# Performance work log

Hardware: AMD Instinct MI355X
Metric: run time of the kernel (lower is better)

Reference implementation:

```python
import jax, jax.numpy as jnp
import numpy as np

P, N, GRID, C, S, STEPS, N_ADJ = 128, 512, 112, 64, 128, 3, 4
HW = GRID * GRID
IN_DIM = C + 2


def _ring_adjacency():
    # prepare_gcn_component builds a ring graph: each vertex connected to
    # n_adj nearest neighbors along the polygon, row-normalized.
    offs = np.concatenate([np.arange(1, N_ADJ // 2 + 1), -np.arange(1, N_ADJ // 2 + 1)])
    A = np.zeros((N, N), np.float32)
    idx = np.arange(N)
    for o in offs:
        A[idx, (idx + o) % N] = 1.0
    A /= A.sum(1, keepdims=True)
    return jnp.asarray(A)


def setup_inputs() -> dict:
    key = jax.random.key(0)
    ks = jax.random.split(key, 10)
    std = 0.01  # matches m.weight.data.normal_(0.0, 0.01)
    return {
        "feature": jax.random.normal(ks[0], (P, HW, C), jnp.float32),
        "init_polys": jax.random.uniform(ks[1], (P, N, 2), jnp.float32),
        "adj": _ring_adjacency(),
        "W1s": jax.random.normal(ks[2], (STEPS, IN_DIM, S), jnp.float32) * std,
        "W1n": jax.random.normal(ks[3], (STEPS, IN_DIM, S), jnp.float32) * std,
        "b1": jnp.zeros((STEPS, S), jnp.float32),
        "W2s": jax.random.normal(ks[4], (STEPS, S, S), jnp.float32) * std,
        "W2n": jax.random.normal(ks[5], (STEPS, S, S), jnp.float32) * std,
        "b2": jnp.zeros((STEPS, S), jnp.float32),
        "Wfc": jax.random.normal(ks[6], (STEPS, S, 2), jnp.float32) * std,
        "bfc": jnp.zeros((STEPS, 2), jnp.float32),
    }


def _gather(feat, ids):
    # feat: [P, HW, C], ids: [P, N] int -> [P, N, C]
    return jnp.take_along_axis(feat, ids[:, :, None], axis=1)


def _nearest_sample(feature, poly):
    # step-0 `sampling` path: gather at floor(coord*grid) flat indices
    X0 = jnp.clip(jnp.floor(poly[..., 0] * GRID), 0, GRID - 1)
    Y0 = jnp.clip(jnp.floor(poly[..., 1] * GRID), 0, GRID - 1)
    ids = (X0 + Y0 * GRID).astype(jnp.int32)
    return _gather(feature, ids)


def _interpolated_sum(feature, poly):
    Xs = poly[..., 0] * GRID
    Ys = poly[..., 1] * GRID
    X0 = jnp.floor(Xs); X1 = X0 + 1.0
    Y0 = jnp.floor(Ys); Y1 = Y0 + 1.0
    w00 = (X1 - Xs) * (Y1 - Ys)
    w01 = (X1 - Xs) * (Ys - Y0)
    w10 = (Xs - X0) * (Y1 - Ys)
    w11 = (Xs - X0) * (Ys - Y0)
    X0c = jnp.clip(X0, 0, GRID - 1).astype(jnp.int32)
    X1c = jnp.clip(X1, 0, GRID - 1).astype(jnp.int32)
    Y0c = jnp.clip(Y0, 0, GRID - 1).astype(jnp.int32)
    Y1c = jnp.clip(Y1, 0, GRID - 1).astype(jnp.int32)
    M00 = _gather(feature, X0c + Y0c * GRID)
    M01 = _gather(feature, X0c + Y1c * GRID)
    M10 = _gather(feature, X1c + Y0c * GRID)
    M11 = _gather(feature, X1c + Y1c * GRID)
    return (w00[..., None] * M00 + w01[..., None] * M01 +
            w10[..., None] * M10 + w11[..., None] * M11)


def _gconv(x, adj, Ws, Wn, b):
    # x: [P, N, D]; adj: [N, N] (shared ring graph)
    nbr = jnp.einsum('nm,pmd->pnd', adj, x)
    return x @ Ws + nbr @ Wn + b


def _gcn(x, adj, i, W1s, W1n, b1, W2s, W2n, b2, Wfc, bfc):
    h = jax.nn.relu(_gconv(x, adj, W1s[i], W1n[i], b1[i]))
    h = jax.nn.relu(_gconv(h, adj, W2s[i], W2n[i], b2[i]))
    return h @ Wfc[i] + bfc[i]  # [P, N, 2]


def reference(feature, init_polys, adj, W1s, W1n, b1, W2s, W2n, b2, Wfc, bfc):
    poly = init_polys
    for i in range(STEPS):
        cnn_feat = _nearest_sample(feature, poly) if i == 0 else _interpolated_sum(feature, poly)
        inp = jnp.concatenate([cnn_feat, poly], axis=2)  # [P, N, C+2]
        pred = _gcn(inp, adj, i, W1s, W1n, b1, W2s, W2n, b2, Wfc, bfc)
        poly = poly + pred
    return poly
```

## Files before the change

### kernel.cpp

```cpp
#include <hip/hip_runtime.h>

#define P_      128
#define NV      512
#define GRID_   112
#define HW_     (GRID_*GRID_)
#define C_      64
#define S_      128

typedef short bf16x8 __attribute__((ext_vector_type(8)));
typedef float f32x4  __attribute__((ext_vector_type(4)));

__device__ __forceinline__ unsigned short f2bf(float x) {
    union { float f; unsigned int u; } v; v.f = x;
    unsigned int r = (v.u + 0x7FFFu + ((v.u >> 16) & 1u)) >> 16;
    return (unsigned short)r;
}
__device__ __forceinline__ float2 up2(unsigned int u) {
    union { unsigned int u; float f; } a, b;
    a.u = u << 16; b.u = u & 0xFFFF0000u;
    return make_float2(a.f, b.f);
}
__device__ __forceinline__ unsigned int pk2(float lo, float hi) {
    return (unsigned int)f2bf(lo) | ((unsigned int)f2bf(hi) << 16);
}

__global__ __launch_bounds__(256) void wprep_kernel(
    const float* __restrict__ W1s, const float* __restrict__ W1n,
    const float* __restrict__ W2s, const float* __restrict__ W2n,
    unsigned short* __restrict__ W1p, unsigned short* __restrict__ W2p)
{
    int idx = blockIdx.x * 256 + threadIdx.x;
    const int N1 = 3 * 5 * 8 * 64 * 8;
    const int N2 = 3 * 8 * 8 * 64 * 8;
    if (idx < N1) {
        int j = idx & 7, lane = (idx >> 3) & 63, nt = (idx >> 9) & 7;
        int ks = (idx >> 12) % 5, step = idx / 20480;
        int n = nt * 16 + (lane & 15);
        int k = ks * 32 + (lane >> 4) * 8 + j;
        float v = 0.f;
        if (k < 66)       v = W1s[(step * 66 + k) * 128 + n];
        else if (k < 132) v = W1n[(step * 66 + (k - 66)) * 128 + n];
        W1p[idx] = f2bf(v);
    } else if (idx < N1 + N2) {
        int e = idx - N1;
        int j = e & 7, lane = (e >> 3) & 63, nt = (e >> 9) & 7;
        int ks = (e >> 12) & 7, step = e >> 15;
        int n = nt * 16 + (lane & 15);
        int k = ks * 32 + (lane >> 4) * 8 + j;
        float v = (k < 128) ? W2s[(step * 128 + k) * 128 + n]
                            : W2n[(step * 128 + (k - 128)) * 128 + n];
        W2p[e] = f2bf(v);
    }
}

__global__ __launch_bounds__(256) void sample_kernel(
    const float* __restrict__ feature, const float* __restrict__ poly,
    unsigned short* __restrict__ inp, int nearest)
{
    int w = threadIdx.x >> 6, lane = threadIdx.x & 63;
    int g = blockIdx.x * 4 + w;
    int p = g >> 9;
    float px = poly[2 * g], py = poly[2 * g + 1];
    const float* fb = feature + (size_t)p * HW_ * C_;
    float val;
    if (nearest) {
        float X0 = fminf(fmaxf(floorf(px * (float)GRID_), 0.f), (float)(GRID_ - 1));
        float Y0 = fminf(fmaxf(floorf(py * (float)GRID_), 0.f), (float)(GRID_ - 1));
        int id = (int)X0 + (int)Y0 * GRID_;
        val = fb[(size_t)id * C_ + lane];
    } else {
        float Xs = px * (float)GRID_, Ys = py * (float)GRID_;
        float X0 = floorf(Xs), Y0 = floorf(Ys);
        float X1 = X0 + 1.f, Y1 = Y0 + 1.f;
        float ax = X1 - Xs, bx = Xs - X0;
        float ay = Y1 - Ys, by = Ys - Y0;
        int X0c = (int)fminf(fmaxf(X0, 0.f), (float)(GRID_ - 1));
        int X1c = (int)fminf(fmaxf(X1, 0.f), (float)(GRID_ - 1));
        int Y0c = (int)fminf(fmaxf(Y0, 0.f), (float)(GRID_ - 1));
        int Y1c = (int)fminf(fmaxf(Y1, 0.f), (float)(GRID_ - 1));
        float m00 = fb[(size_t)(X0c + Y0c * GRID_) * C_ + lane];
        float m01 = fb[(size_t)(X0c + Y1c * GRID_) * C_ + lane];
        float m10 = fb[(size_t)(X1c + Y0c * GRID_) * C_ + lane];
        float m11 = fb[(size_t)(X1c + Y1c * GRID_) * C_ + lane];
        val = (ax * ay) * m00 + (ax * by) * m01 + (bx * ay) * m10 + (bx * by) * m11;
    }
    unsigned short* row = inp + (size_t)g * 72;
    row[lane] = f2bf(val);
    if (lane < 8)
        row[64 + lane] = (lane == 0) ? f2bf(px) : (lane == 1) ? f2bf(py) : 0;
}

__global__ __launch_bounds__(256) void gcn_kernel(
    const unsigned short* __restrict__ inp,
    const unsigned short* __restrict__ W1p,
    const float* __restrict__ b1,
    const unsigned short* __restrict__ W2p,
    const float* __restrict__ b2,
    const float* __restrict__ Wfc, const float* __restrict__ bfc,
    const float* __restrict__ poly_in, float* __restrict__ poly_out)
{
    __shared__ __align__(16) char smem[54400];
    unsigned int*   raw_u = (unsigned int*)smem;
    unsigned int*   A1_u  = (unsigned int*)(smem + 10368);
    unsigned short* h1s   = (unsigned short*)smem;
    unsigned int*   A2_u  = (unsigned int*)(smem + 21120);
    float*          h2    = (float*)(smem + 21120);

    int p = blockIdx.x >> 3, n0 = (blockIdx.x & 7) * 64;
    int wv = threadIdx.x >> 6, lane = threadIdx.x & 63;
    int m = lane & 15, q = lane >> 4;

    const unsigned int* inpu = (const unsigned int*)inp + (size_t)p * NV * 36;
    for (int idx = threadIdx.x; idx < 72 * 36; idx += 256) {
        int r = idx / 36, u = idx - r * 36;
        raw_u[idx] = inpu[(size_t)((n0 + r - 4) & 511) * 36 + u];
    }
    __syncthreads();

    for (int idx = threadIdx.x; idx < 80 * 84; idx += 256) {
        int a = idx / 84, u = idx - a * 84;
        unsigned int val = 0u;
        if (a < 68) {
            if (u < 33) {
                val = raw_u[(a + 2) * 36 + u];
            } else if (u < 66) {
                int uu = u - 33;
                float2 fa = up2(raw_u[a * 36 + uu]),       fb2 = up2(raw_u[(a + 1) * 36 + uu]);
                float2 fc = up2(raw_u[(a + 3) * 36 + uu]), fd  = up2(raw_u[(a + 4) * 36 + uu]);
                val = pk2(0.25f * (fa.x + fb2.x + fc.x + fd.x),
                          0.25f * (fa.y + fb2.y + fc.y + fd.y));
            }
        }
        A1_u[idx] = val;
    }
    __syncthreads();

    f32x4 acc1[10];
    #pragma unroll
    for (int i = 0; i < 10; i++) acc1[i] = (f32x4){0.f, 0.f, 0.f, 0.f};
    const bf16x8* B1 = (const bf16x8*)W1p;
    #pragma unroll
    for (int i = 0; i < 10; i++) {
        int t = wv * 10 + i;
        int mt = t >> 3, nt = t & 7;
        const unsigned short* arow = (const unsigned short*)A1_u + (mt * 16 + m) * 168 + q * 8;
        #pragma unroll
        for (int ks = 0; ks < 5; ks++) {
            bf16x8 a = *(const bf16x8*)(arow + ks * 32);
            bf16x8 b = B1[(ks * 8 + nt) * 64 + lane];
            acc1[i] = __builtin_amdgcn_mfma_f32_16x16x32_bf16(a, b, acc1[i], 0, 0, 0);
        }
    }
    __syncthreads();

    #pragma unroll
    for (int i = 0; i < 10; i++) {
        int t = wv * 10 + i;
        int mt = t >> 3, nt = t & 7;
        int col = nt * 16 + m;
        float bias = b1[col];
        #pragma unroll
        for (int rg = 0; rg < 4; rg++) {
            int row = mt * 16 + q * 4 + rg;
            h1s[row * 132 + col] = f2bf(fmaxf(acc1[i][rg] + bias, 0.f));
        }
    }
    __syncthreads();

    const unsigned int* h1u = (const unsigned int*)h1s;
    for (int idx = threadIdx.x; idx < 64 * 128; idx += 256) {
        int a = idx >> 7, u = idx & 127;
        unsigned int val;
        if (u < 64) {
            val = h1u[(a + 2) * 66 + u];
        } else {
            int uu = u - 64;
            float2 fa = up2(h1u[a * 66 + uu]),       fb2 = up2(h1u[(a + 1) * 66 + uu]);
            float2 fc = up2(h1u[(a + 3) * 66 + uu]), fd  = up2(h1u[(a + 4) * 66 + uu]);
            val = pk2(0.25f * (fa.x + fb2.x + fc.x + fd.x),
                      0.25f * (fa.y + fb2.y + fc.y + fd.y));
        }
        A2_u[a * 130 + u] = val;
    }
    __syncthreads();

    f32x4 acc2[8];
    #pragma unroll
    for (int nt = 0; nt < 8; nt++) acc2[nt] = (f32x4){0.f, 0.f, 0.f, 0.f};
    const bf16x8* B2 = (const bf16x8*)W2p;
    const unsigned short* arow2 = (const unsigned short*)A2_u + (wv * 16 + m) * 260 + q * 8;
    #pragma unroll
    for (int ks = 0; ks < 8; ks++) {
        bf16x8 a = *(const bf16x8*)(arow2 + ks * 32);
        #pragma unroll
        for (int nt = 0; nt < 8; nt++) {
            bf16x8 b = B2[(ks * 8 + nt) * 64 + lane];
            acc2[nt] = __builtin_amdgcn_mfma_f32_16x16x32_bf16(a, b, acc2[nt], 0, 0, 0);
        }
    }
    __syncthreads();

    #pragma unroll
    for (int nt = 0; nt < 8; nt++) {
        int col = nt * 16 + m;
        float bias = b2[col];
        #pragma unroll
        for (int rg = 0; rg < 4; rg++) {
            int row = wv * 16 + q * 4 + rg;
            h2[row * 129 + col] = fmaxf(acc2[nt][rg] + bias, 0.f);
        }
    }
    __syncthreads();

    {
        int t = threadIdx.x;
        int oi = t >> 1, half = t & 1;
        int v = oi >> 1, j = oi & 1;
        float pr = half ? 0.f : bfc[j];
        const float* hv = h2 + v * 129 + half * 64;
        #pragma unroll 8
        for (int cc = 0; cc < 64; cc++)
            pr += hv[cc] * Wfc[(half * 64 + cc) * 2 + j];
        pr += __shfl_xor(pr, 1);
        if (half == 0) {
            size_t o = ((size_t)p * NV + n0 + v) * 2 + j;
            poly_out[o] = poly_in[o] + pr;
        }
    }
}

extern "C" void kernel_launch(void* const* d_in, const int* in_sizes, int n_in,
                              void* d_out, int out_size, void* d_ws, size_t ws_size,
                              hipStream_t stream)
{
    const float* feature    = (const float*)d_in[0];
    const float* init_polys = (const float*)d_in[1];
    const float* W1s = (const float*)d_in[3];
    const float* W1n = (const float*)d_in[4];
    const float* b1  = (const float*)d_in[5];
    const float* W2s = (const float*)d_in[6];
    const float* W2n = (const float*)d_in[7];
    const float* b2  = (const float*)d_in[8];
    const float* Wfc = (const float*)d_in[9];
    const float* bfc = (const float*)d_in[10];
    float* out = (float*)d_out;

    char* wsb = (char*)d_ws;
    float* polyA = (float*)wsb;                  wsb += (size_t)P_ * NV * 2 * 4;
    float* polyB = (float*)wsb;                  wsb += (size_t)P_ * NV * 2 * 4;
    unsigned short* W1p = (unsigned short*)wsb;  wsb += (size_t)61440 * 2;
    unsigned short* W2p = (unsigned short*)wsb;  wsb += (size_t)98304 * 2;
    unsigned short* inp = (unsigned short*)wsb;

    wprep_kernel<<<624, 256, 0, stream>>>(W1s, W1n, W2s, W2n, W1p, W2p);

    const float* pin = init_polys;
    for (int i = 0; i < 3; i++) {
        float* pout = (i == 2) ? out : ((i == 0) ? polyA : polyB);
        sample_kernel<<<P_ * NV / 4, 256, 0, stream>>>(feature, pin, inp, i == 0);
        gcn_kernel<<<P_ * 8, 256, 0, stream>>>(
            inp, W1p + (size_t)i * 20480, b1 + i * 128,
            W2p + (size_t)i * 32768, b2 + i * 128,
            Wfc + i * 256, bfc + i * 2,
            pin, pout);
        pin = pout;
    }
}
```

Measured before the change: 644.7 us.

## Fuse feature sampling into GCN kernel and reorganize MFMA tiling by column pairs

```diff
diff --git a/kernel.cpp b/kernel.cpp
--- a/kernel.cpp
+++ b/kernel.cpp
@@ -53,53 +53,18 @@
     }
 }
 
-__global__ __launch_bounds__(256) void sample_kernel(
-    const float* __restrict__ feature, const float* __restrict__ poly,
-    unsigned short* __restrict__ inp, int nearest)
-{
-    int w = threadIdx.x >> 6, lane = threadIdx.x & 63;
-    int g = blockIdx.x * 4 + w;
-    int p = g >> 9;
-    float px = poly[2 * g], py = poly[2 * g + 1];
-    const float* fb = feature + (size_t)p * HW_ * C_;
-    float val;
-    if (nearest) {
-        float X0 = fminf(fmaxf(floorf(px * (float)GRID_), 0.f), (float)(GRID_ - 1));
-        float Y0 = fminf(fmaxf(floorf(py * (float)GRID_), 0.f), (float)(GRID_ - 1));
-        int id = (int)X0 + (int)Y0 * GRID_;
-        val = fb[(size_t)id * C_ + lane];
-    } else {
-        float Xs = px * (float)GRID_, Ys = py * (float)GRID_;
-        float X0 = floorf(Xs), Y0 = floorf(Ys);
-        float X1 = X0 + 1.f, Y1 = Y0 + 1.f;
-        float ax = X1 - Xs, bx = Xs - X0;
-        float ay = Y1 - Ys, by = Ys - Y0;
-        int X0c = (int)fminf(fmaxf(X0, 0.f), (float)(GRID_ - 1));
-        int X1c = (int)fminf(fmaxf(X1, 0.f), (float)(GRID_ - 1));
-        int Y0c = (int)fminf(fmaxf(Y0, 0.f), (float)(GRID_ - 1));
-        int Y1c = (int)fminf(fmaxf(Y1, 0.f), (float)(GRID_ - 1));
-        float m00 = fb[(size_t)(X0c + Y0c * GRID_) * C_ + lane];
-        float m01 = fb[(size_t)(X0c + Y1c * GRID_) * C_ + lane];
-        float m10 = fb[(size_t)(X1c + Y0c * GRID_) * C_ + lane];
-        float m11 = fb[(size_t)(X1c + Y1c * GRID_) * C_ + lane];
-        val = (ax * ay) * m00 + (ax * by) * m01 + (bx * ay) * m10 + (bx * by) * m11;
-    }
-    unsigned short* row = inp + (size_t)g * 72;
-    row[lane] = f2bf(val);
-    if (lane < 8)
-        row[64 + lane] = (lane == 0) ? f2bf(px) : (lane == 1) ? f2bf(py) : 0;
-}
-
 __global__ __launch_bounds__(256) void gcn_kernel(
-    const unsigned short* __restrict__ inp,
+    const float* __restrict__ feature,
     const unsigned short* __restrict__ W1p,
     const float* __restrict__ b1,
     const unsigned short* __restrict__ W2p,
     const float* __restrict__ b2,
     const float* __restrict__ Wfc, const float* __restrict__ bfc,
-    const float* __restrict__ poly_in, float* __restrict__ poly_out)
+    const float* __restrict__ poly_in, float* __restrict__ poly_out,
+    int nearest)
 {
     __shared__ __align__(16) char smem[54400];
+    unsigned short* rawS  = (unsigned short*)smem;
     unsigned int*   raw_u = (unsigned int*)smem;
     unsigned int*   A1_u  = (unsigned int*)(smem + 10368);
     unsigned short* h1s   = (unsigned short*)smem;
@@ -109,11 +74,41 @@
     int p = blockIdx.x >> 3, n0 = (blockIdx.x & 7) * 64;
     int wv = threadIdx.x >> 6, lane = threadIdx.x & 63;
     int m = lane & 15, q = lane >> 4;
-
-    const unsigned int* inpu = (const unsigned int*)inp + (size_t)p * NV * 36;
-    for (int idx = threadIdx.x; idx < 72 * 36; idx += 256) {
-        int r = idx / 36, u = idx - r * 36;
-        raw_u[idx] = inpu[(size_t)((n0 + r - 4) & 511) * 36 + u];
+    int nt0 = wv * 2;
+
+    const float* fb    = feature + (size_t)p * HW_ * C_;
+    const float* pbase = poly_in + (size_t)p * NV * 2;
+    #pragma unroll 3
+    for (int r = wv; r < 72; r += 4) {
+        int vtx = (n0 + r - 4) & (NV - 1);
+        float px = pbase[2 * vtx], py = pbase[2 * vtx + 1];
+        float val;
+        if (nearest) {
+            float X0 = fminf(fmaxf(floorf(px * (float)GRID_), 0.f), (float)(GRID_ - 1));
+            float Y0 = fminf(fmaxf(floorf(py * (float)GRID_), 0.f), (float)(GRID_ - 1));
+            int id = (int)X0 + (int)Y0 * GRID_;
+            val = fb[(size_t)id * C_ + lane];
+        } else {
+            float Xs = px * (float)GRID_, Ys = py * (float)GRID_;
+            float X0 = floorf(Xs), Y0 = floorf(Ys);
+            float X1 = X0 + 1.f, Y1 = Y0 + 1.f;
+            float ax = X1 - Xs, bx = Xs - X0;
+            float ay = Y1 - Ys, by = Ys - Y0;
+            int X0c = (int)fminf(fmaxf(X0, 0.f), (float)(GRID_ - 1));
+            int X1c = (int)fminf(fmaxf(X1, 0.f), (float)(GRID_ - 1));
+            int Y0c = (int)fminf(fmaxf(Y0, 0.f), (float)(GRID_ - 1));
+            int Y1c = (int)fminf(fmaxf(Y1, 0.f), (float)(GRID_ - 1));
+            float m00 = fb[(size_t)(X0c + Y0c * GRID_) * C_ + lane];
+            float m01 = fb[(size_t)(X0c + Y1c * GRID_) * C_ + lane];
+            float m10 = fb[(size_t)(X1c + Y0c * GRID_) * C_ + lane];
+            float m11 = fb[(size_t)(X1c + Y1c * GRID_) * C_ + lane];
+            val = (ax * ay) * m00 + (ax * by) * m01 + (bx * ay) * m10 + (bx * by) * m11;
+        }
+        unsigned short* row = rawS + r * 72;
+        row[lane] = f2bf(val);
+        if (lane < 8)
+            row[64 + lane] = (lane == 0) ? f2bf(px) : (lane == 1) ? f2bf(py)
+                                                                  : (unsigned short)0;
     }
     __syncthreads();
 
@@ -135,34 +130,38 @@
     }
     __syncthreads();
 
-    f32x4 acc1[10];
-    #pragma unroll
-    for (int i = 0; i < 10; i++) acc1[i] = (f32x4){0.f, 0.f, 0.f, 0.f};
+    f32x4 acc1[5][2];
+    #pragma unroll
+    for (int i = 0; i < 5; i++) {
+        acc1[i][0] = (f32x4){0.f, 0.f, 0.f, 0.f};
+        acc1[i][1] = (f32x4){0.f, 0.f, 0.f, 0.f};
+    }
     const bf16x8* B1 = (const bf16x8*)W1p;
-    #pragma unroll
-    for (int i = 0; i < 10; i++) {
-        int t = wv * 10 + i;
-        int mt = t >> 3, nt = t & 7;
-        const unsigned short* arow = (const unsigned short*)A1_u + (mt * 16 + m) * 168 + q * 8;
-        #pragma unroll
-        for (int ks = 0; ks < 5; ks++) {
-            bf16x8 a = *(const bf16x8*)(arow + ks * 32);
-            bf16x8 b = B1[(ks * 8 + nt) * 64 + lane];
-            acc1[i] = __builtin_amdgcn_mfma_f32_16x16x32_bf16(a, b, acc1[i], 0, 0, 0);
-        }
-    }
-    __syncthreads();
-
-    #pragma unroll
-    for (int i = 0; i < 10; i++) {
-        int t = wv * 10 + i;
-        int mt = t >> 3, nt = t & 7;
-        int col = nt * 16 + m;
-        float bias = b1[col];
-        #pragma unroll
-        for (int rg = 0; rg < 4; rg++) {
-            int row = mt * 16 + q * 4 + rg;
-            h1s[row * 132 + col] = f2bf(fmaxf(acc1[i][rg] + bias, 0.f));
+    const unsigned short* A1s = (const unsigned short*)A1_u;
+    #pragma unroll
+    for (int ks = 0; ks < 5; ks++) {
+        bf16x8 bfr0 = B1[(ks * 8 + nt0) * 64 + lane];
+        bf16x8 bfr1 = B1[(ks * 8 + nt0 + 1) * 64 + lane];
+        #pragma unroll
+        for (int mt = 0; mt < 5; mt++) {
+            bf16x8 a = *(const bf16x8*)(A1s + (mt * 16 + m) * 168 + ks * 32 + q * 8);
+            acc1[mt][0] = __builtin_amdgcn_mfma_f32_16x16x32_bf16(a, bfr0, acc1[mt][0], 0, 0, 0);
+            acc1[mt][1] = __builtin_amdgcn_mfma_f32_16x16x32_bf16(a, bfr1, acc1[mt][1], 0, 0, 0);
+        }
+    }
+    __syncthreads();
+
+    #pragma unroll
+    for (int mt = 0; mt < 5; mt++) {
+        #pragma unroll
+        for (int j = 0; j < 2; j++) {
+            int col = (nt0 + j) * 16 + m;
+            float bias = b1[col];
+            #pragma unroll
+            for (int rg = 0; rg < 4; rg++) {
+                int row = mt * 16 + q * 4 + rg;
+                h1s[row * 132 + col] = f2bf(fmaxf(acc1[mt][j][rg] + bias, 0.f));
+            }
         }
     }
     __syncthreads();
@@ -184,30 +183,38 @@
     }
     __syncthreads();
 
-    f32x4 acc2[8];
-    #pragma unroll
-    for (int nt = 0; nt < 8; nt++) acc2[nt] = (f32x4){0.f, 0.f, 0.f, 0.f};
+    f32x4 acc2[4][2];
+    #pragma unroll
+    for (int i = 0; i < 4; i++) {
+        acc2[i][0] = (f32x4){0.f, 0.f, 0.f, 0.f};
+        acc2[i][1] = (f32x4){0.f, 0.f, 0.f, 0.f};
+    }
     const bf16x8* B2 = (const bf16x8*)W2p;
-    const unsigned short* arow2 = (const unsigned short*)A2_u + (wv * 16 + m) * 260 + q * 8;
+    const unsigned short* A2s = (const unsigned short*)A2_u;
     #pragma unroll
     for (int ks = 0; ks < 8; ks++) {
-        bf16x8 a = *(const bf16x8*)(arow2 + ks * 32);
-        #pragma unroll
-        for (int nt = 0; nt < 8; nt++) {
-            bf16x8 b = B2[(ks * 8 + nt) * 64 + lane];
-            acc2[nt] = __builtin_amdgcn_mfma_f32_16x16x32_bf16(a, b, acc2[nt], 0, 0, 0);
-        }
-    }
-    __syncthreads();
-
-    #pragma unroll
-    for (int nt = 0; nt < 8; nt++) {
-        int col = nt * 16 + m;
-        float bias = b2[col];
-        #pragma unroll
-        for (int rg = 0; rg < 4; rg++) {
-            int row = wv * 16 + q * 4 + rg;
-            h2[row * 129 + col] = fmaxf(acc2[nt][rg] + bias, 0.f);
+        bf16x8 bfr0 = B2[(ks * 8 + nt0) * 64 + lane];
+        bf16x8 bfr1 = B2[(ks * 8 + nt0 + 1) * 64 + lane];
+        #pragma unroll
+        for (int mt = 0; mt < 4; mt++) {
+            bf16x8 a = *(const bf16x8*)(A2s + (mt * 16 + m) * 260 + ks * 32 + q * 8);
+            acc2[mt][0] = __builtin_amdgcn_mfma_f32_16x16x32_bf16(a, bfr0, acc2[mt][0], 0, 0, 0);
+            acc2[mt][1] = __builtin_amdgcn_mfma_f32_16x16x32_bf16(a, bfr1, acc2[mt][1], 0, 0, 0);
+        }
+    }
+    __syncthreads();
+
+    #pragma unroll
+    for (int mt = 0; mt < 4; mt++) {
+        #pragma unroll
+        for (int j = 0; j < 2; j++) {
+            int col = (nt0 + j) * 16 + m;
+            float bias = b2[col];
+            #pragma unroll
+            for (int rg = 0; rg < 4; rg++) {
+                int row = mt * 16 + q * 4 + rg;
+                h2[row * 129 + col] = fmaxf(acc2[mt][j][rg] + bias, 0.f);
+            }
         }
     }
     __syncthreads();
@@ -249,20 +256,19 @@
     float* polyA = (float*)wsb;                  wsb += (size_t)P_ * NV * 2 * 4;
     float* polyB = (float*)wsb;                  wsb += (size_t)P_ * NV * 2 * 4;
     unsigned short* W1p = (unsigned short*)wsb;  wsb += (size_t)61440 * 2;
-    unsigned short* W2p = (unsigned short*)wsb;  wsb += (size_t)98304 * 2;
-    unsigned short* inp = (unsigned short*)wsb;
+    unsigned short* W2p = (unsigned short*)wsb;
 
     wprep_kernel<<<624, 256, 0, stream>>>(W1s, W1n, W2s, W2n, W1p, W2p);
 
     const float* pin = init_polys;
     for (int i = 0; i < 3; i++) {
         float* pout = (i == 2) ? out : ((i == 0) ? polyA : polyB);
-        sample_kernel<<<P_ * NV / 4, 256, 0, stream>>>(feature, pin, inp, i == 0);
         gcn_kernel<<<P_ * 8, 256, 0, stream>>>(
-            inp, W1p + (size_t)i * 20480, b1 + i * 128,
+            feature,
+            W1p + (size_t)i * 20480, b1 + i * 128,
             W2p + (size_t)i * 32768, b2 + i * 128,
             Wfc + i * 256, bfc + i * 2,
-            pin, pout);
+            pin, pout, i == 0);
         pin = pout;
     }
 }
```

After: 692.6 us. +7.4%, slower.
